# Kernel tuning notes

Hardware: AMD Instinct MI355X
Metric: run time of the kernel (lower is better)

The kernel has to match this reference:

```python
import jax, jax.numpy as jnp
import numpy as np

D_MODEL = 768
HEADS = 4
HEAD_DIM = D_MODEL // HEADS
SCALE = 20.0  # source divides scores by hard-coded 20
NEG = -1e9
LN_EPS = 1e-5


def setup_inputs() -> dict:
    key = jax.random.key(0)
    ks = jax.random.split(key, 8)
    B, S = 4, 2048
    x = jax.random.normal(ks[0], (B, S, D_MODEL), dtype=jnp.float32)
    attention_mask = jnp.zeros((B, 1, S), dtype=bool)  # no padding
    s = 1.0 / np.sqrt(D_MODEL)
    Wq = jax.random.normal(ks[1], (D_MODEL, D_MODEL), dtype=jnp.float32) * s
    Wk = jax.random.normal(ks[2], (D_MODEL, D_MODEL), dtype=jnp.float32) * s
    Wv = jax.random.normal(ks[3], (D_MODEL, D_MODEL), dtype=jnp.float32) * s
    bq = jnp.zeros((D_MODEL,), jnp.float32)
    bk = jnp.zeros((D_MODEL,), jnp.float32)
    bv = jnp.zeros((D_MODEL,), jnp.float32)
    gamma = jnp.ones((D_MODEL,), jnp.float32)
    beta = jnp.zeros((D_MODEL,), jnp.float32)
    return {"x": x, "attention_mask": attention_mask, "Wq": Wq, "bq": bq,
            "Wk": Wk, "bk": bk, "Wv": Wv, "bv": bv, "gamma": gamma, "beta": beta}


def _split_heads(t, B, S):
    return t.reshape(B, S, HEADS, HEAD_DIM).transpose(0, 2, 1, 3)  # [B,H,S,D]


def reference(x, attention_mask, Wq, bq, Wk, bk, Wv, bv, gamma, beta):
    B, S, _ = x.shape
    Q = _split_heads(x @ Wq.T + bq, B, S)
    K = _split_heads(x @ Wk.T + bk, B, S)
    V = _split_heads(x @ Wv.T + bv, B, S)
    # scores [B,H,Sq,Sk]
    w = jnp.einsum('bhqd,bhkd->bhqk', Q, K) / SCALE
    pad = attention_mask[:, :, :, None]                     # [B,1,S,1] -> broadcast
    look = jnp.triu(jnp.ones((S, S), dtype=bool), 1)        # strict upper triangle
    mask = look[None, None] | pad
    w = jnp.where(mask, NEG, w)
    # NOTE: source uses Softmax(dim=2), i.e. over the QUERY axis — kept faithfully
    attn = jax.nn.softmax(w, axis=2)
    x1 = jnp.einsum('bhqk,bhkd->bhqd', attn, V)             # [B,H,S,D]
    x1 = x1.transpose(0, 2, 1, 3).reshape(B, S, D_MODEL)
    y = x + x1
    mu = jnp.mean(y, axis=-1, keepdims=True)
    var = jnp.mean((y - mu) ** 2, axis=-1, keepdims=True)
    return (y - mu) * jax.lax.rsqrt(var + LN_EPS) * gamma + beta
```

## Files before the change

kernel.cpp:

```cpp
#include <hip/hip_runtime.h>

typedef _Float16 f16;
typedef _Float16 f16x8 __attribute__((ext_vector_type(8)));
typedef _Float16 f16x4 __attribute__((ext_vector_type(4)));
typedef float    f32x4 __attribute__((ext_vector_type(4)));

#define MFMA16(a,b,c) __builtin_amdgcn_mfma_f32_16x16x32_f16(a,b,c,0,0,0)

static constexpr float NEGV = -1e9f;
static constexpr float SC   = 0.05f;


__device__ __forceinline__ int poff(int qt){
    int m = qt>>1;
    return qt + m*(m-1) + ((qt&1) ? m : 0);
}

__device__ __forceinline__ void gload16(const void* g, void* l){
    __builtin_amdgcn_global_load_lds(
        (const __attribute__((address_space(1))) void*)g,
        (__attribute__((address_space(3))) void*)l, 16, 0, 0);
}

__global__ __launch_bounds__(256) void cvt_kernel(const float* __restrict__ in,
                                                  f16* __restrict__ out, int n){
    int i = (blockIdx.x*256 + threadIdx.x)*4;
    if (i < n){
        float4 v = *reinterpret_cast<const float4*>(in + i);
        f16x4 o = { (f16)v.x, (f16)v.y, (f16)v.z, (f16)v.w };
        *reinterpret_cast<f16x4*>(out + i) = o;
    }
}

__global__ __launch_bounds__(256) void cvtw_kernel(const float* __restrict__ a,
                                                   const float* __restrict__ b,
                                                   const float* __restrict__ c,
                                                   f16* __restrict__ out){
    int idx = blockIdx.x*256 + threadIdx.x;
    int which = idx / 147456;
    int r = idx - which*147456;
    const float* src = (which==0) ? a : (which==1 ? b : c);
    int i = r*4;
    float4 v = *reinterpret_cast<const float4*>(src + i);
    f16x4 o = { (f16)v.x, (f16)v.y, (f16)v.z, (f16)v.w };
    *reinterpret_cast<f16x4*>(out + (size_t)which*589824 + i) = o;
}

__global__ __launch_bounds__(256) void zero_kernel(float* __restrict__ p, int n){
    int i = (blockIdx.x*256 + threadIdx.x)*4;
    if (i < n){
        float4 z = {0.f,0.f,0.f,0.f};
        *reinterpret_cast<float4*>(p + i) = z;
    }
}

__global__ __launch_bounds__(256) void proj_kernel(
    const f16* __restrict__ xb, const f16* __restrict__ Wb,
    const float* __restrict__ bq, const float* __restrict__ bk, const float* __restrict__ bv,
    f16* __restrict__ Qb, f16* __restrict__ Kb, f16* __restrict__ Vt)
{
    __shared__ f16 As[128*32];
    __shared__ f16 Bs[128*32];
    const int z = blockIdx.z;
    const f16*   Wz   = Wb + (size_t)z*768*768;
    const float* bias = (z==0) ? bq : (z==1 ? bk : bv);
    f16*         out  = (z==0) ? Qb : (z==1 ? Kb : Vt);
    const int row0 = blockIdx.y*128, n0 = blockIdx.x*128;
    const int tid = threadIdx.x, w = tid>>6, l = tid&63;
    const int wm = w>>1, wn = w&1, c = l&15, g = l>>4;
    f32x4 zero = {0.f,0.f,0.f,0.f};
    f32x4 acc[4][4];
    for (int i=0;i<4;i++) for (int j=0;j<4;j++) acc[i][j] = zero;

    const f16* ag = xb + (size_t)(row0 + w*32 + (l>>2))*768 + (l&3)*8;
    const f16* bg = Wz + (size_t)(n0   + w*32 + (l>>2))*768 + (l&3)*8;
    f16* asd = As + w*1024;
    f16* bsd = Bs + w*1024;

    for (int k0 = 0; k0 < 768; k0 += 32){
        __syncthreads();
        gload16(ag + k0,          asd      );
        gload16(ag + k0 + 16*768, asd + 512);
        gload16(bg + k0,          bsd      );
        gload16(bg + k0 + 16*768, bsd + 512);
        __syncthreads();
        f16x8 af[4], bf[4];
        for (int mt=0; mt<4; mt++)
            af[mt] = *reinterpret_cast<const f16x8*>(As + (wm*64 + mt*16 + c)*32 + g*8);
        for (int nt=0; nt<4; nt++)
            bf[nt] = *reinterpret_cast<const f16x8*>(Bs + (wn*64 + nt*16 + c)*32 + g*8);
        for (int mt=0; mt<4; mt++)
            for (int nt=0; nt<4; nt++)
                acc[mt][nt] = MFMA16(af[mt], bf[nt], acc[mt][nt]);
    }

    for (int nt=0; nt<4; nt++){
        int nb = n0 + wn*64 + nt*16;
        int h  = nb/192;
        int d  = (nb - h*192) + c;
        float bv_ = bias[nb + c];
        for (int mt=0; mt<4; mt++){
            int mb = row0 + wm*64 + mt*16 + g*4;
            int bi = mb>>11, s0 = mb&2047;
            int bh = bi*4 + h;
            if (z < 2){
                int ds = d>>5, gg = (d>>3)&3, e = d&7;
                for (int r=0;r<4;r++){
                    int s = s0 + r;
                    out[ ((size_t)(bh*128 + (s>>4))*6 + ds)*512 + ((gg*16) + (s&15))*8 + e ]
                        = (f16)(acc[mt][nt][r] + bv_);
                }
            } else {
                int dt = d>>4, cV = d&15;
                int kb64 = s0>>6, ks = (s0>>5)&1, gk = (s0>>3)&3, e0 = s0&7;
                f16x4 pk = { (f16)(acc[mt][nt][0] + bv_), (f16)(acc[mt][nt][1] + bv_),
                             (f16)(acc[mt][nt][2] + bv_), (f16)(acc[mt][nt][3] + bv_) };
                *reinterpret_cast<f16x4*>(
                    &out[ ((size_t)(bh*32 + kb64)*24 + dt*2 + ks)*512 + (gk*16 + cV)*8 + e0 ]) = pk;
            }
        }
    }
}

__global__ __launch_bounds__(512,4) void qkexp_kernel(
    const f16* __restrict__ Qb, const f16* __restrict__ Kb,
    const unsigned char* __restrict__ am,
    float* __restrict__ L, f16* __restrict__ Pg)
{
    __shared__ f16 Ks[2][24*512];
    __shared__ f16 Pl[8][16*32];
    const int bh = blockIdx.z, b = bh>>2;
    const int qb = blockIdx.x;
    const int ch = blockIdx.y;
    if (qb < 4*ch) return;
    const int tid = threadIdx.x, w = tid>>6, l = tid&63;
    const int c = l&15, g = l>>4;
    const int qt = qb*8 + w, qw = qt*16;
    const f16* Kfm = Kb + (size_t)bh*128*6*512;
    char* Pb = (char*)(&Pl[w][0]);
    f16* pw = Pg + ((size_t)bh*4160 + poff(qt))*512 + l*8;
    float* Lb = L + bh*2048;

    f16x8 qf[6];
    {
        const f16* qbase = Qb + ((size_t)(bh*128 + qt)*6)*512 + l*8;
        for (int ds=0; ds<6; ds++) qf[ds] = *reinterpret_cast<const f16x8*>(qbase + ds*512);
    }
    bool pm[4];
    for (int r=0;r<4;r++) pm[r] = am[b*2048 + qw + g*4 + r] != 0;

    f32x4 zero = {0.f,0.f,0.f,0.f};
    const int k00  = ch*512;
    const int kend = min(ch*512 + 512, qb*128 + 128);
    const int nt   = (kend - k00) >> 6;
    const int cid  = w*3;

    auto stage = [&](int buf, int k0){
        for (int i=0;i<3;i++){
            int ci = cid + i;
            int tl = ci/6, ds = ci - tl*6;
            gload16(Kfm + ((size_t)((k0>>4) + tl)*6 + ds)*512 + l*8, &Ks[buf][ci*512]);
        }
    };

    stage(0, k00);
    __syncthreads();
    for (int it=0; it<nt; it++){
        int cur = it&1;
        int k0  = k00 + it*64;
        if (it+1 < nt) stage(cur^1, k0 + 64);

        for (int half=0; half<2; half++){
            int kh = k0 + half*32;
            if (kh <= qw + 15){
                float cs[2];
                for (int kt2=0; kt2<2; kt2++){
                    int ktile = half*2 + kt2;
                    int kk = k0 + ktile*16;
                    f32x4 sacc = zero;
                    for (int ds=0; ds<6; ds++){
                        f16x8 kfr = *reinterpret_cast<const f16x8*>(&Ks[cur][(ktile*6+ds)*512 + l*8]);
                        sacc = MFMA16(qf[ds], kfr, sacc);
                    }
                    float csl = 0.f;
                    for (int r=0;r<4;r++){
                        int q = qw + g*4 + r;
                        float v = sacc[r]*SC;
                        if (pm[r]) v = NEGV;
                        float p = __expf(v);
                        if (kk + c > q) p = 0.f;
                        csl += p;
                        int row = g*4 + r;
                        int byo = (row*64 + (kt2*16 + c)*2) ^ ((row&3)<<4);
                        *reinterpret_cast<f16*>(Pb + byo) = (f16)p;
                    }
                    csl += __shfl_xor(csl, 16);
                    csl += __shfl_xor(csl, 32);
                    cs[kt2] = csl;
                }
                {
                    int byo = (c*64 + g*16) ^ ((c&3)<<4);
                    f16x8 pa = *reinterpret_cast<const f16x8*>(Pb + byo);
                    *reinterpret_cast<f16x8*>(pw + (size_t)(kh>>5)*512) = pa;
                }
                if (l < 32){
                    float csv = (l < 16) ? cs[0] : cs[1];
                    int kcol = kh + ((l < 16) ? 0 : 16) + (l & 15);
                    atomicAdd(&Lb[kcol], csv);
                }
            }
        }
        __syncthreads();
    }
}

__global__ __launch_bounds__(256) void scalev_kernel(f16* __restrict__ V, const float* __restrict__ L){
    int idx = blockIdx.x*256 + threadIdx.x;
    size_t base = (size_t)idx * 8;
    int bh = idx / 49152;
    int rem = idx - bh*49152;
    int chunk = rem >> 6;
    int sl = rem & 63;
    int kb64 = chunk/24, cr = chunk - kb64*24;
    int ks = cr & 1;
    int gk = sl >> 4;
    int k0 = kb64*64 + ks*32 + gk*8;
    const float* Lb = L + bh*2048 + k0;
    f16x8 v = *reinterpret_cast<f16x8*>(V + base);
    f16x8 o;
    for (int e=0;e<8;e++){
        float Lv = fmaxf(Lb[e], 1e-30f);
        o[e] = (f16)((float)v[e] / Lv);
    }
    *reinterpret_cast<f16x8*>(V + base) = o;
}

__global__ __launch_bounds__(512,4) void pv_kernel(
    const f16* __restrict__ Pg, const f16* __restrict__ Vt,
    float* __restrict__ x1)
{
    __shared__ f16 Vs[2][12*512];
    const int bh = blockIdx.z, b = bh>>2, h = bh&3;
    const int qb = blockIdx.x;
    const int ch = blockIdx.y;
    if (qb < 4*ch) return;
    const int tid = threadIdx.x, w = tid>>6, l = tid&63;
    const int c = l&15, g = l>>4;
    const int qt = qb*8 + w, qw = qt*16;
    const f16* Vfm = Vt + (size_t)bh*32*24*512;
    const f16* pp  = Pg + ((size_t)bh*4160 + poff(qt))*512 + l*8;

    f32x4 zero = {0.f,0.f,0.f,0.f};
    f32x4 acc[12];
    for (int i=0;i<12;i++) acc[i] = zero;

    const int k00  = ch*512;
    const int kend = min(ch*512 + 512, qb*128 + 128);
    const int nt   = (kend - k00) >> 5;
    const int cid  = w*3;

    auto stage = [&](int buf, int k0){
        for (int i=0;i<3;i++){
            int ci = cid + i;
            if (ci < 12)
                gload16(Vfm + ((size_t)(k0>>6)*24 + ci*2 + ((k0>>5)&1))*512 + l*8, &Vs[buf][ci*512]);
        }
    };

    stage(0, k00);
    f16x8 pa_cur = *reinterpret_cast<const f16x8*>(pp + (size_t)(k00>>5)*512);
    __syncthreads();
    for (int it=0; it<nt; it++){
        int cur = it&1;
        int k0  = k00 + it*32;
        if (it+1 < nt) stage(cur^1, k0 + 32);

        f16x8 pa_next = pa_cur;
        bool actn = (it+1 < nt) && (k0 + 32 <= qw + 15);
        if (actn) pa_next = *reinterpret_cast<const f16x8*>(pp + (size_t)((k0+32)>>5)*512);

        if (k0 <= qw + 15){
            for (int dt=0; dt<12; dt++){
                f16x8 vb = *reinterpret_cast<const f16x8*>(&Vs[cur][dt*512 + l*8]);
                acc[dt] = MFMA16(pa_cur, vb, acc[dt]);
            }
        }
        __syncthreads();
        pa_cur = pa_next;
    }
    for (int dt=0; dt<12; dt++){
        int d = h*192 + dt*16 + c;
        for (int r=0;r<4;r++){
            int q = qw + g*4 + r;
            atomicAdd(&x1[(size_t)(b*2048 + q)*768 + d], acc[dt][r]);
        }
    }
}

__global__ __launch_bounds__(256) void ln_kernel(
    const float* __restrict__ x, const float* __restrict__ x1,
    const float* __restrict__ gamma, const float* __restrict__ beta,
    float* __restrict__ out)
{
    const int r = blockIdx.x, t = threadIdx.x;
    const float* xr = x  + (size_t)r*768;
    const float* yr = x1 + (size_t)r*768;
    float v[3]; float s1 = 0.f, s2 = 0.f;
    for (int i=0;i<3;i++){ int j = t + i*256; float y = xr[j] + yr[j]; v[i]=y; s1+=y; s2+=y*y; }
    for (int o=32;o>=1;o>>=1){ s1 += __shfl_xor(s1,o); s2 += __shfl_xor(s2,o); }
    __shared__ float a1[4], a2[4];
    if ((t&63)==0){ a1[t>>6]=s1; a2[t>>6]=s2; }
    __syncthreads();
    s1 = a1[0]+a1[1]+a1[2]+a1[3];
    s2 = a2[0]+a2[1]+a2[2]+a2[3];
    float mu  = s1*(1.f/768.f);
    float var = s2*(1.f/768.f) - mu*mu;
    float rs  = rsqrtf(var + 1e-5f);
    for (int i=0;i<3;i++){
        int j = t + i*256;
        out[(size_t)r*768 + j] = (v[i]-mu)*rs*gamma[j] + beta[j];
    }
}

extern "C" void kernel_launch(void* const* d_in, const int* in_sizes, int n_in,
                              void* d_out, int out_size, void* d_ws, size_t ws_size,
                              hipStream_t stream)
{
    const float* x     = (const float*)d_in[0];
    const unsigned char* am = (const unsigned char*)d_in[1];
    const float* Wq    = (const float*)d_in[2];
    const float* bq    = (const float*)d_in[3];
    const float* Wk    = (const float*)d_in[4];
    const float* bk    = (const float*)d_in[5];
    const float* Wv    = (const float*)d_in[6];
    const float* bv    = (const float*)d_in[7];
    const float* gamma = (const float*)d_in[8];
    const float* beta  = (const float*)d_in[9];
    float* out = (float*)d_out;

    f16* xb  = (f16*)d_ws;
    f16* Wb  = xb + (size_t)8192*768;
    f16* Qb  = Wb + (size_t)3*768*768;
    f16* Kb  = Qb + (size_t)16*2048*192;
    f16* Vt  = Kb + (size_t)16*2048*192;
    f16* Pg  = Vt + (size_t)16*2048*192;
    float* L  = (float*)xb;
    float* x1 = (float*)Qb;

    cvt_kernel<<<6144, 256, 0, stream>>>(x,  xb, 8192*768);
    cvtw_kernel<<<1728, 256, 0, stream>>>(Wq, Wk, Wv, Wb);
    proj_kernel<<<dim3(6,64,3), 256, 0, stream>>>(xb, Wb, bq, bk, bv, Qb, Kb, Vt);
    zero_kernel<<<32, 256, 0, stream>>>(L, 16*2048);
    qkexp_kernel<<<dim3(16,4,16), 512, 0, stream>>>(Qb, Kb, am, L, Pg);
    zero_kernel<<<6144, 256, 0, stream>>>(x1, 8192*768);
    scalev_kernel<<<3072, 256, 0, stream>>>(Vt, L);
    pv_kernel<<<dim3(16,4,16), 512, 0, stream>>>(Pg, Vt, x1);
    ln_kernel<<<8192, 256, 0, stream>>>(x, x1, gamma, beta, out);
}
```

Measured before the change: 301.2 us.

## Restructure PV kernel to per-wave full-K with direct stores; double-buffer projection GEMM

The PV kernel no longer splits K into chunks across blocks. Each wave now owns one 16-row query tile and half the head dimension and walks the whole causal K range, reading V straight from global memory instead of staging it in LDS. Query tiles are paired short-with-long to balance work, results are written with plain stores, and the x1 zeroing kernel and atomics are removed. Separately, the projection GEMM double-buffers its LDS tiles so the next K-slice loads while the current one is used, with one barrier per iteration instead of two. The risks are more global V traffic without LDS reuse across waves, and uneven per-wave work in the PV kernel.

```diff
diff --git a/kernel.cpp b/kernel.cpp
--- a/kernel.cpp
+++ b/kernel.cpp
@@ -59,8 +59,8 @@
     const float* __restrict__ bq, const float* __restrict__ bk, const float* __restrict__ bv,
     f16* __restrict__ Qb, f16* __restrict__ Kb, f16* __restrict__ Vt)
 {
-    __shared__ f16 As[128*32];
-    __shared__ f16 Bs[128*32];
+    __shared__ f16 As[2][128*32];
+    __shared__ f16 Bs[2][128*32];
     const int z = blockIdx.z;
     const f16*   Wz   = Wb + (size_t)z*768*768;
     const float* bias = (z==0) ? bq : (z==1 ? bk : bv);
@@ -74,24 +74,28 @@
 
     const f16* ag = xb + (size_t)(row0 + w*32 + (l>>2))*768 + (l&3)*8;
     const f16* bg = Wz + (size_t)(n0   + w*32 + (l>>2))*768 + (l&3)*8;
-    f16* asd = As + w*1024;
-    f16* bsd = Bs + w*1024;
-
-    for (int k0 = 0; k0 < 768; k0 += 32){
-        __syncthreads();
-        gload16(ag + k0,          asd      );
-        gload16(ag + k0 + 16*768, asd + 512);
-        gload16(bg + k0,          bsd      );
-        gload16(bg + k0 + 16*768, bsd + 512);
-        __syncthreads();
+
+    auto stage = [&](int buf, int k0){
+        gload16(ag + k0,          &As[buf][w*1024      ]);
+        gload16(ag + k0 + 16*768, &As[buf][w*1024 + 512]);
+        gload16(bg + k0,          &Bs[buf][w*1024      ]);
+        gload16(bg + k0 + 16*768, &Bs[buf][w*1024 + 512]);
+    };
+
+    stage(0, 0);
+    __syncthreads();
+    for (int it=0; it<24; it++){
+        int cur = it&1;
+        if (it < 23) stage(cur^1, (it+1)*32);
         f16x8 af[4], bf[4];
         for (int mt=0; mt<4; mt++)
-            af[mt] = *reinterpret_cast<const f16x8*>(As + (wm*64 + mt*16 + c)*32 + g*8);
+            af[mt] = *reinterpret_cast<const f16x8*>(&As[cur][(wm*64 + mt*16 + c)*32 + g*8]);
         for (int nt=0; nt<4; nt++)
-            bf[nt] = *reinterpret_cast<const f16x8*>(Bs + (wn*64 + nt*16 + c)*32 + g*8);
+            bf[nt] = *reinterpret_cast<const f16x8*>(&Bs[cur][(wn*64 + nt*16 + c)*32 + g*8]);
         for (int mt=0; mt<4; mt++)
             for (int nt=0; nt<4; nt++)
                 acc[mt][nt] = MFMA16(af[mt], bf[nt], acc[mt][nt]);
+        __syncthreads();
     }
 
     for (int nt=0; nt<4; nt++){
@@ -235,64 +239,59 @@
     *reinterpret_cast<f16x8*>(V + base) = o;
 }
 
-__global__ __launch_bounds__(512,4) void pv_kernel(
+__global__ __launch_bounds__(512) void pv_kernel(
     const f16* __restrict__ Pg, const f16* __restrict__ Vt,
     float* __restrict__ x1)
 {
-    __shared__ f16 Vs[2][12*512];
-    const int bh = blockIdx.z, b = bh>>2, h = bh&3;
-    const int qb = blockIdx.x;
-    const int ch = blockIdx.y;
-    if (qb < 4*ch) return;
-    const int tid = threadIdx.x, w = tid>>6, l = tid&63;
-    const int c = l&15, g = l>>4;
-    const int qt = qb*8 + w, qw = qt*16;
+    const int t  = blockIdx.x*8 + (threadIdx.x>>6);
+    const int l  = threadIdx.x&63, c = l&15, g = l>>4;
+    const int bh = t >> 8;
+    const int r8 = t & 255;
+    const int dh = r8 & 1;
+    const int j  = r8 >> 1;
+    const int qt = (j&1) ? (127 - (j>>1)) : (j>>1);
+    const int b = bh>>2, h = bh&3;
+    const int qw = qt*16;
     const f16* Vfm = Vt + (size_t)bh*32*24*512;
     const f16* pp  = Pg + ((size_t)bh*4160 + poff(qt))*512 + l*8;
+    const int nc = (qt>>1) + 1;
 
     f32x4 zero = {0.f,0.f,0.f,0.f};
-    f32x4 acc[12];
-    for (int i=0;i<12;i++) acc[i] = zero;
-
-    const int k00  = ch*512;
-    const int kend = min(ch*512 + 512, qb*128 + 128);
-    const int nt   = (kend - k00) >> 5;
-    const int cid  = w*3;
-
-    auto stage = [&](int buf, int k0){
-        for (int i=0;i<3;i++){
-            int ci = cid + i;
-            if (ci < 12)
-                gload16(Vfm + ((size_t)(k0>>6)*24 + ci*2 + ((k0>>5)&1))*512 + l*8, &Vs[buf][ci*512]);
-        }
-    };
-
-    stage(0, k00);
-    f16x8 pa_cur = *reinterpret_cast<const f16x8*>(pp + (size_t)(k00>>5)*512);
-    __syncthreads();
-    for (int it=0; it<nt; it++){
-        int cur = it&1;
-        int k0  = k00 + it*32;
-        if (it+1 < nt) stage(cur^1, k0 + 32);
-
-        f16x8 pa_next = pa_cur;
-        bool actn = (it+1 < nt) && (k0 + 32 <= qw + 15);
-        if (actn) pa_next = *reinterpret_cast<const f16x8*>(pp + (size_t)((k0+32)>>5)*512);
-
-        if (k0 <= qw + 15){
-            for (int dt=0; dt<12; dt++){
-                f16x8 vb = *reinterpret_cast<const f16x8*>(&Vs[cur][dt*512 + l*8]);
-                acc[dt] = MFMA16(pa_cur, vb, acc[dt]);
-            }
-        }
-        __syncthreads();
-        pa_cur = pa_next;
-    }
-    for (int dt=0; dt<12; dt++){
-        int d = h*192 + dt*16 + c;
+    f32x4 acc[6];
+    for (int i=0;i<6;i++) acc[i] = zero;
+
+    int kc = 0;
+    for (; kc+1 < nc; kc += 2){
+        const f16* pap = pp + (size_t)kc*512;
+        f16x8 paA = *reinterpret_cast<const f16x8*>(pap);
+        f16x8 paB = *reinterpret_cast<const f16x8*>(pap + 512);
+        const f16* vb = Vfm + ((size_t)(kc>>1)*24 + dh*12)*512 + l*8;
+        f16x8 vA[6], vB[6];
+        #pragma unroll
+        for (int d2=0; d2<6; d2++){
+            vA[d2] = *reinterpret_cast<const f16x8*>(vb + d2*1024);
+            vB[d2] = *reinterpret_cast<const f16x8*>(vb + d2*1024 + 512);
+        }
+        #pragma unroll
+        for (int d2=0; d2<6; d2++) acc[d2] = MFMA16(paA, vA[d2], acc[d2]);
+        #pragma unroll
+        for (int d2=0; d2<6; d2++) acc[d2] = MFMA16(paB, vB[d2], acc[d2]);
+    }
+    if (kc < nc){
+        f16x8 paA = *reinterpret_cast<const f16x8*>(pp + (size_t)kc*512);
+        const f16* vb = Vfm + ((size_t)(kc>>1)*24 + dh*12)*512 + l*8;
+        #pragma unroll
+        for (int d2=0; d2<6; d2++){
+            f16x8 vA = *reinterpret_cast<const f16x8*>(vb + d2*1024);
+            acc[d2] = MFMA16(paA, vA, acc[d2]);
+        }
+    }
+
+    for (int d2=0; d2<6; d2++){
+        int d = h*192 + (dh*6 + d2)*16 + c;
         for (int r=0;r<4;r++){
             int q = qw + g*4 + r;
-            atomicAdd(&x1[(size_t)(b*2048 + q)*768 + d], acc[dt][r]);
+            x1[(size_t)(b*2048 + q)*768 + d] = acc[d2][r];
         }
     }
 }
@@ -352,8 +351,7 @@
     proj_kernel<<<dim3(6,64,3), 256, 0, stream>>>(xb, Wb, bq, bk, bv, Qb, Kb, Vt);
     zero_kernel<<<32, 256, 0, stream>>>(L, 16*2048);
     qkexp_kernel<<<dim3(16,4,16), 512, 0, stream>>>(Qb, Kb, am, L, Pg);
-    zero_kernel<<<6144, 256, 0, stream>>>(x1, 8192*768);
     scalev_kernel<<<3072, 256, 0, stream>>>(Vt, L);
-    pv_kernel<<<dim3(16,4,16), 512, 0, stream>>>(Pg, Vt, x1);
+    pv_kernel<<<512, 512, 0, stream>>>(Pg, Vt, x1);
     ln_kernel<<<8192, 256, 0, stream>>>(x, x1, gamma, beta, out);
 }
```

Result: faster. 282.4 us (-6.2%).
